# Performance work log

Hardware: AMD Instinct MI355X
Metric: run time of the kernel (lower is better)

The kernel has to match this reference:

```python
import jax, jax.numpy as jnp
import numpy as np

D_MODEL = 1024
D_FF = 4096
NUM_HEADS = 16
D_HEAD = D_MODEL // NUM_HEADS
EPS = 1e-5


def setup_inputs() -> dict:
    key = jax.random.key(0)
    ks = jax.random.split(key, 16)
    s = 0.02
    return {
        "X": jax.random.normal(ks[0], (2, 2048, D_MODEL), dtype=jnp.float32),
        "W_qkv": jax.random.normal(ks[1], (D_MODEL, 3 * D_MODEL), dtype=jnp.float32) * s,
        "b_qkv": jax.random.normal(ks[2], (3 * D_MODEL,), dtype=jnp.float32) * s,
        "W_o": jax.random.normal(ks[3], (D_MODEL, D_MODEL), dtype=jnp.float32) * s,
        "b_o": jax.random.normal(ks[4], (D_MODEL,), dtype=jnp.float32) * s,
        "W_1": jax.random.normal(ks[5], (D_MODEL, D_FF), dtype=jnp.float32) * s,
        "b_1": jax.random.normal(ks[6], (D_FF,), dtype=jnp.float32) * s,
        "W_2": jax.random.normal(ks[7], (D_FF, D_MODEL), dtype=jnp.float32) * s,
        "b_2": jax.random.normal(ks[8], (D_MODEL,), dtype=jnp.float32) * s,
        "ln1_g": jnp.ones((D_MODEL,), dtype=jnp.float32),
        "ln1_b": jnp.zeros((D_MODEL,), dtype=jnp.float32),
        "ln2_g": jnp.ones((D_MODEL,), dtype=jnp.float32),
        "ln2_b": jnp.zeros((D_MODEL,), dtype=jnp.float32),
    }


def _layernorm(x, g, b):
    mu = jnp.mean(x, axis=-1, keepdims=True)
    var = jnp.mean(jnp.square(x - mu), axis=-1, keepdims=True)
    return (x - mu) * jax.lax.rsqrt(var + EPS) * g + b


def reference(X, W_qkv, b_qkv, W_o, b_o, W_1, b_1, W_2, b_2, ln1_g, ln1_b, ln2_g, ln2_b):
    B, T, D = X.shape
    qkv = X @ W_qkv + b_qkv                      # [B,T,3D]
    Q, K, V = jnp.split(qkv, 3, axis=-1)
    # [B,H,T,d]
    Q = Q.reshape(B, T, NUM_HEADS, D_HEAD).transpose(0, 2, 1, 3)
    K = K.reshape(B, T, NUM_HEADS, D_HEAD).transpose(0, 2, 1, 3)
    V = V.reshape(B, T, NUM_HEADS, D_HEAD).transpose(0, 2, 1, 3)
    scores = jnp.einsum('bhqd,bhkd->bhqk', Q, K) / np.float32(D_HEAD) ** 0.5
    causal = jnp.tril(jnp.ones((T, T), dtype=bool))
    scores = jnp.where(causal, scores, jnp.float32(-jnp.inf))
    A = jax.nn.softmax(scores, axis=-1)
    O = jnp.einsum('bhqk,bhkd->bhqd', A, V)
    O = O.transpose(0, 2, 1, 3).reshape(B, T, D)
    O = O @ W_o + b_o
    H_1 = _layernorm(X + O, ln1_g, ln1_b)
    H_2 = (jax.nn.gelu(H_1 @ W_1 + b_1, approximate=False)) @ W_2 + b_2
    return _layernorm(H_1 + H_2, ln2_g, ln2_b)
```

## Files before the change

### kernel.cpp

```cpp
#include <hip/hip_runtime.h>
#include <cmath>

typedef unsigned short u16;
typedef __bf16 bf16x8 __attribute__((ext_vector_type(8)));
typedef float f32x4 __attribute__((ext_vector_type(4)));

#define DEVI __device__ __forceinline__

DEVI float b2f(u16 u){ union{unsigned int i; float f;} v; v.i=(unsigned int)u<<16; return v.f; }
DEVI u16 f2b(float f){ union{unsigned int i; float f;} v; v.f=f;
    unsigned int r=(v.i+0x7FFFu+((v.i>>16)&1u))>>16; return (u16)r; }

DEVI void gload_lds16(const u16* g, u16* l){
    __builtin_amdgcn_global_load_lds((__attribute__((address_space(1))) void*)g,
                                     (__attribute__((address_space(3))) void*)l,
                                     16, 0, 0);
}

__global__ __launch_bounds__(256)
void cvt_bf16(const float* __restrict__ in, u16* __restrict__ out)
{
    const int i = (blockIdx.x * 256 + threadIdx.x) * 4;
    float4 v = *(const float4*)&in[i];
    ushort4 o;
    o.x = f2b(v.x); o.y = f2b(v.y); o.z = f2b(v.z); o.w = f2b(v.w);
    *(ushort4*)&out[i] = o;
}

__global__ __launch_bounds__(256)
void cvt_transpose(const float* __restrict__ in, u16* __restrict__ out, int R, int C)
{
    __shared__ __align__(16) u16 tile[64*72];
    const int rb = blockIdx.x*64, cb = blockIdx.y*64;
    const int t = threadIdx.x;
    const int r = t >> 3, c0 = (t & 7) * 8;
    #pragma unroll
    for (int rr = 0; rr < 2; rr++) {
        const int row = r + rr*32;
        float4 a = *(const float4*)&in[(long)(rb + row)*C + cb + c0];
        float4 b = *(const float4*)&in[(long)(rb + row)*C + cb + c0 + 4];
        u16* tp = &tile[row*72 + c0];
        tp[0]=f2b(a.x); tp[1]=f2b(a.y); tp[2]=f2b(a.z); tp[3]=f2b(a.w);
        tp[4]=f2b(b.x); tp[5]=f2b(b.y); tp[6]=f2b(b.z); tp[7]=f2b(b.w);
    }
    __syncthreads();
    #pragma unroll
    for (int rr = 0; rr < 2; rr++) {
        const int cr = r + rr*32;
        u16 tmp[8];
        #pragma unroll
        for (int j = 0; j < 8; j++) tmp[j] = tile[(c0 + j)*72 + cr];
        *(uint4*)&out[(long)(cb + cr)*R + rb + c0] = *(uint4*)tmp;
    }
}

template<int EPI, int BM, int DBUF>
__global__ __launch_bounds__(256)
void gemm_bt(const u16* __restrict__ A, const u16* __restrict__ Bt,
             const float* __restrict__ bias, const u16* __restrict__ Res,
             u16* __restrict__ C, u16* __restrict__ C2, int M, int N, int K)
{
    constexpr int RM = BM / 32;
    constexpr int NA = (BM / 16) * 2 / 4;
    constexpr int ASZ = BM*64, BSZ = 128*64;
    __shared__ __align__(16) u16 As[(DBUF ? 2 : 1)*ASZ];
    __shared__ __align__(16) u16 Bs[(DBUF ? 2 : 1)*BSZ];
    const int tid  = threadIdx.x;
    const int wave = tid >> 6, lane = tid & 63;
    const int tm = blockIdx.x * BM, tn = blockIdx.y * 128;

    const int rs = lane >> 2, cs = ((lane & 3) ^ ((lane >> 3) & 3)) * 8;
    const u16* gA[NA]; u16* lA[NA];
    #pragma unroll
    for (int i = 0; i < NA; i++) {
        const int c = wave + i*4;
        const int p = c / (BM/16), rb = c % (BM/16);
        gA[i] = A + (long)(tm + rb*16 + rs)*K + p*32 + cs;
        lA[i] = As + p*(BM*32) + rb*512;
    }
    const u16* gB[4]; u16* lB[4];
    #pragma unroll
    for (int i = 0; i < 4; i++) {
        const int c = wave + i*4;
        const int p = c >> 3, rb = c & 7;
        gB[i] = Bt + (long)(tn + rb*16 + rs)*K + p*32 + cs;
        lB[i] = Bs + p*(128*32) + rb*512;
    }

    const int wm = (wave >> 1) * (BM/2), wn = (wave & 1) * 64;
    const int fr = lane & 15, fq = lane >> 4;
    const int fs = (fq ^ ((fr >> 1) & 3)) * 8;

    f32x4 acc[RM][4] = {};

    if constexpr (DBUF) {
        const int nk = K >> 6;
        #pragma unroll
        for (int i = 0; i < NA; i++) gload_lds16(gA[i], lA[i]);
        #pragma unroll
        for (int i = 0; i < 4; i++)  gload_lds16(gB[i], lB[i]);
        for (int t = 0; t < nk; t++) {
            __syncthreads();
            if (t + 1 < nk) {
                const int nb = (t + 1) & 1;
                const int k0 = (t + 1) << 6;
                #pragma unroll
                for (int i = 0; i < NA; i++) gload_lds16(gA[i] + k0, lA[i] + nb*ASZ);
                #pragma unroll
                for (int i = 0; i < 4; i++)  gload_lds16(gB[i] + k0, lB[i] + nb*BSZ);
            }
            const u16* Ab = As + (t & 1)*ASZ;
            const u16* Bb = Bs + (t & 1)*BSZ;
            #pragma unroll
            for (int p = 0; p < 2; p++) {
                bf16x8 af[RM], bfr[4];
                #pragma unroll
                for (int i = 0; i < RM; i++)
                    af[i]  = *(const bf16x8*)&Ab[p*(BM*32) + (wm + i*16 + fr)*32 + fs];
                #pragma unroll
                for (int j = 0; j < 4; j++)
                    bfr[j] = *(const bf16x8*)&Bb[p*(128*32) + (wn + j*16 + fr)*32 + fs];
                #pragma unroll
                for (int i = 0; i < RM; i++)
                    #pragma unroll
                    for (int j = 0; j < 4; j++)
                        acc[i][j] = __builtin_amdgcn_mfma_f32_16x16x32_bf16(af[i], bfr[j], acc[i][j], 0, 0, 0);
            }
        }
    } else {
        for (int k0 = 0; k0 < K; k0 += 64) {
            __syncthreads();
            #pragma unroll
            for (int i = 0; i < NA; i++) gload_lds16(gA[i] + k0, lA[i]);
            #pragma unroll
            for (int i = 0; i < 4; i++)  gload_lds16(gB[i] + k0, lB[i]);
            __syncthreads();
            #pragma unroll
            for (int p = 0; p < 2; p++) {
                bf16x8 af[RM], bfr[4];
                #pragma unroll
                for (int i = 0; i < RM; i++)
                    af[i]  = *(const bf16x8*)&As[p*(BM*32) + (wm + i*16 + fr)*32 + fs];
                #pragma unroll
                for (int j = 0; j < 4; j++)
                    bfr[j] = *(const bf16x8*)&Bs[p*(128*32) + (wn + j*16 + fr)*32 + fs];
                #pragma unroll
                for (int i = 0; i < RM; i++)
                    #pragma unroll
                    for (int j = 0; j < 4; j++)
                        acc[i][j] = __builtin_amdgcn_mfma_f32_16x16x32_bf16(af[i], bfr[j], acc[i][j], 0, 0, 0);
            }
        }
    }

    #pragma unroll
    for (int i = 0; i < RM; i++) {
        const int row = tm + wm + i*16 + fq*4;
        #pragma unroll
        for (int j = 0; j < 4; j++) {
            const int col = tn + wn + j*16 + fr;
            const float bv = bias[col];
            if (EPI == 3 && col >= 2048) {
                const int hh = (col - 2048) >> 6, dd = (col - 2048) & 63;
                const int batch = row >> 11, tok = row & 2047;
                u16 pk[4];
                #pragma unroll
                for (int r = 0; r < 4; r++) pk[r] = f2b(acc[i][j][r] + bv);
                *(uint2*)&C2[((long)(batch*16 + hh)*64 + dd)*2048 + tok] = *(uint2*)pk;
            } else {
                const int cw = (EPI == 3) ? 2048 : N;
                #pragma unroll
                for (int r = 0; r < 4; r++) {
                    float v = acc[i][j][r] + bv;
                    const long idx = (long)(row + r)*cw + col;
                    if (EPI == 1) v += b2f(Res[idx]);
                    if (EPI == 2) {
                        const float u = v + 0.044715f*v*v*v;
                        const float t = exp2f(u * 2.302208f);
                        v = v * t * __builtin_amdgcn_rcpf(t + 1.f);
                    }
                    C[idx] = f2b(v);
                }
            }
        }
    }
}

__global__ __launch_bounds__(512)
void attn_kernel(const u16* __restrict__ QK, const u16* __restrict__ VT,
                 u16* __restrict__ O)
{
    constexpr float CS = 0.18033688011112042f;
    __shared__ __align__(16) u16 smem[40960];

    const int tid = threadIdx.x, wave = tid >> 6, lane = tid & 63;
    const int grp = wave >> 2, wg = wave & 3;
    const int pair = blockIdx.x, h = blockIdx.y, b = blockIdx.z;
    const int fr = lane & 15, fq = lane >> 4;
    const long qkbase = (long)b*2048*2048;
    const long vtbase = (long)(b*16 + h)*64*2048;
    const int rs = lane >> 2, cs2 = ((lane & 3) ^ ((lane >> 3) & 3)) * 8;
    const int fs = (fq ^ ((fr >> 1) & 3)) * 8;
    const int sw = (fr & 7) * 8;
    const int KsBase = grp*8192;
    const int VsBase = 16384 + grp*8192;
    u16* pw = &smem[32768 + wave*1024];

    #define ISSUE(bf, k0)                                                      \
        _Pragma("unroll")                                                      \
        for (int i = 0; i < 2; i++) {                                          \
            const int c = wg + i*4;                                            \
            const int kp = c >> 2, krb = c & 3;                                \
            gload_lds16(QK + qkbase + (long)((k0) + krb*16 + rs)*2048          \
                           + 1024 + h*64 + kp*32 + cs2,                        \
                        &smem[KsBase + (bf)*4096 + kp*2048 + krb*512]);        \
            const int vp = c & 1, vrb = c >> 1;                                \
            gload_lds16(VT + vtbase + (long)(vrb*16 + rs)*2048                 \
                           + (k0) + vp*32 + cs2,                               \
                        &smem[VsBase + (bf)*4096 + vp*2048 + vrb*512]);        \
        }

    #pragma unroll 1
    for (int which = 0; which < 2; which++) {
        const int qt = which ? pair : (31 - pair);

        bf16x8 bq[2];
        #pragma unroll
        for (int ks = 0; ks < 2; ks++)
            bq[ks] = *(const bf16x8*)&QK[qkbase + (long)(qt*64 + wg*16 + fr)*2048
                                         + h*64 + ks*32 + fq*8];

        const int q_glob = qt*64 + wg*16 + fr;
        const int q_wmin = qt*64 + wg*16;
        f32x4 o[4] = {};
        float m_i = -1e30f, l_i = 0.f;
        const int nkt = qt + 1;
        const int nit = (nkt + 1) >> 1;
        const int myn = (nkt + 1 - grp) >> 1;

        if (which) __syncthreads();
        if (grp < nkt) { ISSUE(0, grp*64) }

        for (int it = 0; it < nit; it++) {
            const int kt = 2*it + grp;
            const int k0 = kt * 64;
            const int cur = it & 1;
            __syncthreads();
            if (kt + 2 < nkt) { ISSUE(cur ^ 1, k0 + 128) }

            if (it < myn) {
                f32x4 st[4];
                #pragma unroll
                for (int mt = 0; mt < 4; mt++) st[mt] = (f32x4){0.f,0.f,0.f,0.f};
                #pragma unroll
                for (int mt = 0; mt < 4; mt++)
                    #pragma unroll
                    for (int ks = 0; ks < 2; ks++) {
                        bf16x8 ak = *(const bf16x8*)&smem[KsBase + cur*4096 + ks*2048 + (mt*16 + fr)*32 + fs];
                        st[mt] = __builtin_amdgcn_mfma_f32_16x16x32_bf16(ak, bq[ks], st[mt], 0, 0, 0);
                    }

                float mx = -1e30f;
                if (k0 + 63 > q_wmin) {
                    #pragma unroll
                    for (int mt = 0; mt < 4; mt++)
                        #pragma unroll
                        for (int r = 0; r < 4; r++) {
                            const int key = k0 + mt*16 + fq*4 + r;
                            float v = st[mt][r];
                            if (key > q_glob) v = -1e30f;
                            st[mt][r] = v;
                            mx = fmaxf(mx, v);
                        }
                } else {
                    #pragma unroll
                    for (int mt = 0; mt < 4; mt++)
                        #pragma unroll
                        for (int r = 0; r < 4; r++) mx = fmaxf(mx, st[mt][r]);
                }
                mx = fmaxf(mx, __shfl_xor(mx, 16, 64));
                mx = fmaxf(mx, __shfl_xor(mx, 32, 64));

                if (mx > m_i + 44.357f) {
                    const float alpha = exp2f((m_i - mx) * CS);
                    #pragma unroll
                    for (int dt = 0; dt < 4; dt++)
                        #pragma unroll
                        for (int r = 0; r < 4; r++) o[dt][r] *= alpha;
                    l_i *= alpha;
                    m_i = mx;
                }
                const float nms = -m_i * CS;
                float ps = 0.f;
                #pragma unroll
                for (int mt = 0; mt < 4; mt++)
                    #pragma unroll
                    for (int r = 0; r < 4; r++) {
                        const float p = exp2f(fmaf(st[mt][r], CS, nms));
                        st[mt][r] = p; ps += p;
                    }
                ps += __shfl_xor(ps, 16, 64);
                ps += __shfl_xor(ps, 32, 64);
                l_i += ps;

                #pragma unroll
                for (int mt = 0; mt < 4; mt++)
                    #pragma unroll
                    for (int d = 0; d < 2; d++) {
                        unsigned pk;
                        asm("v_cvt_pk_bf16_f32 %0, %1, %2"
                            : "=v"(pk) : "v"(st[mt][2*d]), "v"(st[mt][2*d+1]));
                        *(unsigned*)&pw[fr*64 + ((mt*16 + fq*4 + 2*d) ^ sw)] = pk;
                    }
                __asm__ volatile("" ::: "memory");
                bf16x8 bp[2];
                #pragma unroll
                for (int kk = 0; kk < 2; kk++)
                    bp[kk] = *(const bf16x8*)&pw[fr*64 + ((kk*32 + fq*8) ^ sw)];
                #pragma unroll
                for (int dt = 0; dt < 4; dt++)
                    #pragma unroll
                    for (int kk = 0; kk < 2; kk++) {
                        bf16x8 av = *(const bf16x8*)&smem[VsBase + cur*4096 + kk*2048 + (dt*16 + fr)*32 + fs];
                        o[dt] = __builtin_amdgcn_mfma_f32_16x16x32_bf16(av, bp[kk], o[dt], 0, 0, 0);
                    }
                __asm__ volatile("" ::: "memory");
            }
        }

        __syncthreads();
        float* MB = (float*)&smem[8192];
        float* ML = (float*)&smem[24576];
        if (grp == 1) {
            #pragma unroll
            for (int dt = 0; dt < 4; dt++)
                *(f32x4*)&MB[(wg*64 + lane)*16 + dt*4] = o[dt];
            if (fq == 0) {
                ML[(wg*16 + fr)*2]     = m_i;
                ML[(wg*16 + fr)*2 + 1] = l_i;
            }
        }
        __syncthreads();
        if (grp == 0) {
            const float m1 = ML[(wg*16 + fr)*2];
            const float l1 = ML[(wg*16 + fr)*2 + 1];
            const float m  = fmaxf(m_i, m1);
            const float e0 = exp2f((m_i - m) * CS);
            const float e1 = exp2f((m1  - m) * CS);
            const float rl = __builtin_amdgcn_rcpf(l_i*e0 + l1*e1);
            const long orow = (long)b*2048 + qt*64 + wg*16 + fr;
            #pragma unroll
            for (int dt = 0; dt < 4; dt++) {
                f32x4 o1 = *(const f32x4*)&MB[(wg*64 + lane)*16 + dt*4];
                u16 pk[4];
                #pragma unroll
                for (int r = 0; r < 4; r++)
                    pk[r] = f2b((o[dt][r]*e0 + o1[r]*e1) * rl);
                *(uint2*)&O[orow*1024 + h*64 + dt*16 + fq*4] = *(uint2*)pk;
            }
        }
    }
    #undef ISSUE
}

template<int OUTF32>
__global__ __launch_bounds__(256)
void ln_kernel(const u16* __restrict__ X, const float* __restrict__ G,
               const float* __restrict__ B, void* __restrict__ Yv)
{
    __shared__ float red[8];
    const int tid = threadIdx.x;
    const long row = blockIdx.x;
    const u16* x = X + row*1024;
    ushort4 u = *(const ushort4*)&x[tid*4];
    const float v0 = b2f(u.x), v1 = b2f(u.y), v2 = b2f(u.z), v3 = b2f(u.w);
    float s = v0+v1+v2+v3;
    float q = v0*v0+v1*v1+v2*v2+v3*v3;
    #pragma unroll
    for (int off = 32; off >= 1; off >>= 1) {
        s += __shfl_xor(s, off, 64);
        q += __shfl_xor(q, off, 64);
    }
    const int wv = tid >> 6;
    if ((tid & 63) == 0) { red[wv*2] = s; red[wv*2+1] = q; }
    __syncthreads();
    s = red[0]+red[2]+red[4]+red[6];
    q = red[1]+red[3]+red[5]+red[7];
    const float mu = s * (1.f/1024.f);
    const float rstd = rsqrtf(fmaxf(q*(1.f/1024.f) - mu*mu, 0.f) + 1e-5f);
    float4 g4 = *(const float4*)&G[tid*4];
    float4 b4 = *(const float4*)&B[tid*4];
    const float y0 = (v0-mu)*rstd*g4.x + b4.x;
    const float y1 = (v1-mu)*rstd*g4.y + b4.y;
    const float y2 = (v2-mu)*rstd*g4.z + b4.z;
    const float y3 = (v3-mu)*rstd*g4.w + b4.w;
    if (OUTF32) {
        float4 o = make_float4(y0, y1, y2, y3);
        *(float4*)&((float*)Yv)[row*1024 + tid*4] = o;
    } else {
        ushort4 o;
        o.x = f2b(y0); o.y = f2b(y1); o.z = f2b(y2); o.w = f2b(y3);
        *(ushort4*)&((u16*)Yv)[row*1024 + tid*4] = o;
    }
}

extern "C" void kernel_launch(void* const* d_in, const int* in_sizes, int n_in,
                              void* d_out, int out_size, void* d_ws, size_t ws_size,
                              hipStream_t stream)
{
    const float* X    = (const float*)d_in[0];
    const float* Wqkv = (const float*)d_in[1];
    const float* bqkv = (const float*)d_in[2];
    const float* Wo   = (const float*)d_in[3];
    const float* bo   = (const float*)d_in[4];
    const float* W1   = (const float*)d_in[5];
    const float* b1   = (const float*)d_in[6];
    const float* W2   = (const float*)d_in[7];
    const float* b2   = (const float*)d_in[8];
    const float* g1   = (const float*)d_in[9];
    const float* be1  = (const float*)d_in[10];
    const float* g2   = (const float*)d_in[11];
    const float* be2  = (const float*)d_in[12];
    float* out = (float*)d_out;

    char* ws = (char*)d_ws;
    u16* Xbf   = (u16*)(ws + 0);
    u16* WqkvT = (u16*)(ws + 8388608);
    u16* WoT   = (u16*)(ws + 14680064);
    u16* QK    = (u16*)(ws + 16777216);
    u16* VT    = (u16*)(ws + 33554432);
    u16* AO    = (u16*)(ws + 41943040);
    u16* S1    = (u16*)(ws + 16777216);
    u16* H1    = (u16*)(ws + 0);
    u16* Gbuf  = (u16*)(ws + 8388608);
    u16* S2    = (u16*)(ws + 41943040);
    u16* W1T   = (u16*)d_out;
    u16* W2T   = (u16*)d_out + 4194304;

    cvt_bf16<<<4096, 256, 0, stream>>>(X, Xbf);
    cvt_transpose<<<dim3(16, 48), 256, 0, stream>>>(Wqkv, WqkvT, 1024, 3072);
    cvt_transpose<<<dim3(16, 16), 256, 0, stream>>>(Wo,   WoT,   1024, 1024);
    cvt_transpose<<<dim3(16, 64), 256, 0, stream>>>(W1,   W1T,   1024, 4096);
    cvt_transpose<<<dim3(64, 16), 256, 0, stream>>>(W2,   W2T,   4096, 1024);

    gemm_bt<3,128,0><<<dim3(32, 24), 256, 0, stream>>>(Xbf, WqkvT, bqkv, nullptr, QK, VT, 4096, 3072, 1024);
    attn_kernel<<<dim3(16, 16, 2), 512, 0, stream>>>(QK, VT, AO);
    gemm_bt<1,128,1><<<dim3(32, 8), 256, 0, stream>>>(AO, WoT, bo, Xbf, S1, nullptr, 4096, 1024, 1024);
    ln_kernel<0><<<4096, 256, 0, stream>>>(S1, g1, be1, H1);
    gemm_bt<2,128,0><<<dim3(32, 32), 256, 0, stream>>>(H1, W1T, b1, nullptr, Gbuf, nullptr, 4096, 4096, 1024);
    gemm_bt<1,128,1><<<dim3(32, 8), 256, 0, stream>>>(Gbuf, W2T, b2, H1, S2, nullptr, 4096, 1024, 4096);
    ln_kernel<1><<<4096, 256, 0, stream>>>(S2, g2, be2, out);
}
```

Measured before the change: 365.4 us.

## Use triple-buffered LDS pipeline with explicit vmcnt waits in N=1024 GEMMs

Replaces the double-buffered K loop in the two N=1024 GEMMs (W_o and W_2) with a three-stage LDS ring buffer. Loads are prefetched two tiles ahead, and completion is tracked with explicit s_waitcnt vmcnt immediates plus a raw s_barrier instead of __syncthreads. The aim is to hide more global-load latency in these low-occupancy 256-block launches. The cost is 50% more LDS per block, and correctness depends on the hardcoded count of 8 loads per thread per stage.

```diff
diff --git a/kernel.cpp b/kernel.cpp
--- a/kernel.cpp
+++ b/kernel.cpp
@@ -54,7 +54,7 @@
     }
 }
 
-template<int EPI, int BM, int DBUF>
+template<int EPI, int BM, int PIPE>
 __global__ __launch_bounds__(256)
 void gemm_bt(const u16* __restrict__ A, const u16* __restrict__ Bt,
              const float* __restrict__ bias, const u16* __restrict__ Res,
@@ -63,8 +63,9 @@
     constexpr int RM = BM / 32;
     constexpr int NA = (BM / 16) * 2 / 4;
     constexpr int ASZ = BM*64, BSZ = 128*64;
-    __shared__ __align__(16) u16 As[(DBUF ? 2 : 1)*ASZ];
-    __shared__ __align__(16) u16 Bs[(DBUF ? 2 : 1)*BSZ];
+    constexpr int NBUF = (PIPE == 2) ? 3 : 1;
+    __shared__ __align__(16) u16 As[NBUF*ASZ];
+    __shared__ __align__(16) u16 Bs[NBUF*BSZ];
     const int tid  = threadIdx.x;
     const int wave = tid >> 6, lane = tid & 63;
     const int tm = blockIdx.x * BM, tn = blockIdx.y * 128;
@@ -93,24 +94,33 @@
 
     f32x4 acc[RM][4] = {};
 
-    if constexpr (DBUF) {
+    if constexpr (PIPE == 2) {
+        static_assert(NA + 4 == 8, "vmcnt immediates assume 8 loads/thread/stage");
         const int nk = K >> 6;
         #pragma unroll
         for (int i = 0; i < NA; i++) gload_lds16(gA[i], lA[i]);
         #pragma unroll
         for (int i = 0; i < 4; i++)  gload_lds16(gB[i], lB[i]);
+        #pragma unroll
+        for (int i = 0; i < NA; i++) gload_lds16(gA[i] + 64, lA[i] + ASZ);
+        #pragma unroll
+        for (int i = 0; i < 4; i++)  gload_lds16(gB[i] + 64, lB[i] + BSZ);
+        int bc = 0;
         for (int t = 0; t < nk; t++) {
-            __syncthreads();
-            if (t + 1 < nk) {
-                const int nb = (t + 1) & 1;
-                const int k0 = (t + 1) << 6;
-                #pragma unroll
-                for (int i = 0; i < NA; i++) gload_lds16(gA[i] + k0, lA[i] + nb*ASZ);
-                #pragma unroll
-                for (int i = 0; i < 4; i++)  gload_lds16(gB[i] + k0, lB[i] + nb*BSZ);
-            }
-            const u16* Ab = As + (t & 1)*ASZ;
-            const u16* Bb = Bs + (t & 1)*BSZ;
+            if (t + 1 < nk) asm volatile("s_waitcnt vmcnt(8)" ::: "memory");
+            else            asm volatile("s_waitcnt vmcnt(0)" ::: "memory");
+            __builtin_amdgcn_s_barrier();
+            __builtin_amdgcn_sched_barrier(0);
+            if (t + 2 < nk) {
+                int bn = bc + 2; if (bn >= 3) bn -= 3;
+                const int k0 = (t + 2) << 6;
+                #pragma unroll
+                for (int i = 0; i < NA; i++) gload_lds16(gA[i] + k0, lA[i] + bn*ASZ);
+                #pragma unroll
+                for (int i = 0; i < 4; i++)  gload_lds16(gB[i] + k0, lB[i] + bn*BSZ);
+            }
+            const u16* Ab = As + bc*ASZ;
+            const u16* Bb = Bs + bc*BSZ;
             #pragma unroll
             for (int p = 0; p < 2; p++) {
                 bf16x8 af[RM], bfr[4];
@@ -126,6 +136,7 @@
                     for (int j = 0; j < 4; j++)
                         acc[i][j] = __builtin_amdgcn_mfma_f32_16x16x32_bf16(af[i], bfr[j], acc[i][j], 0, 0, 0);
             }
+            bc++; if (bc >= 3) bc = 0;
         }
     } else {
         for (int k0 = 0; k0 < K; k0 += 64) {
@@ -445,9 +456,9 @@
 
     gemm_bt<3,128,0><<<dim3(32, 24), 256, 0, stream>>>(Xbf, WqkvT, bqkv, nullptr, QK, VT, 4096, 3072, 1024);
     attn_kernel<<<dim3(16, 16, 2), 512, 0, stream>>>(QK, VT, AO);
-    gemm_bt<1,128,1><<<dim3(32, 8), 256, 0, stream>>>(AO, WoT, bo, Xbf, S1, nullptr, 4096, 1024, 1024);
+    gemm_bt<1,128,2><<<dim3(32, 8), 256, 0, stream>>>(AO, WoT, bo, Xbf, S1, nullptr, 4096, 1024, 1024);
     ln_kernel<0><<<4096, 256, 0, stream>>>(S1, g1, be1, H1);
     gemm_bt<2,128,0><<<dim3(32, 32), 256, 0, stream>>>(H1, W1T, b1, nullptr, Gbuf, nullptr, 4096, 4096, 1024);
-    gemm_bt<1,128,1><<<dim3(32, 8), 256, 0, stream>>>(Gbuf, W2T, b2, H1, S2, nullptr, 4096, 1024, 4096);
+    gemm_bt<1,128,2><<<dim3(32, 8), 256, 0, stream>>>(Gbuf, W2T, b2, H1, S2, nullptr, 4096, 1024, 4096);
     ln_kernel<1><<<4096, 256, 0, stream>>>(S2, g2, be2, out);
 }
```

New measurement: 359.1 us. No clear change (-1.7%).
